# Optimization experiments

Measured on AMD Instinct MI355X. Metric: run time of the kernel, lower is better.

## Reference

```python
import jax, jax.numpy as jnp
import numpy as np

EMB = 512
HEADS = 8
HD = EMB // HEADS
DEPTH = 6
CONT = 100
CAT_DIMS = [100] * 28
CAT = len(CAT_DIMS)
HID = int(EMB * (4.0 / 3.0))  # 682, FT-Transformer ReGLU hidden
B = 128
OFFSETS = jnp.asarray(np.concatenate([[0], np.cumsum(CAT_DIMS[:-1])]).astype(np.int32))
SQRT_EMB = float(np.sqrt(EMB))  # scores are DIVIDED by emb**-0.5 in the source


def setup_inputs() -> dict:
    key = jax.random.key(0)
    ks = jax.random.split(key, 16)
    s = 0.02
    x_cat = jax.random.randint(ks[0], (B, CAT), 0, CAT_DIMS[0]).astype(jnp.float32)
    x_cont = jax.random.normal(ks[1], (B, CONT), dtype=jnp.float32)
    x = jnp.concatenate([x_cat, x_cont], axis=1)  # [B, CAT+CONT]
    return {
        "x": x,
        "tok_w": jax.random.normal(ks[2], (CONT + 1, EMB)) * s,
        "tok_b": jax.random.normal(ks[3], (CONT + CAT, EMB)) * s,
        "cat_emb": jax.random.normal(ks[4], (sum(CAT_DIMS), EMB)) * s,
        "Wqkv": jax.random.normal(ks[5], (DEPTH, EMB, 3 * EMB)) * s,
        "bqkv": jnp.zeros((DEPTH, 3 * EMB)),
        "Wout": jax.random.normal(ks[6], (DEPTH, EMB, EMB)) * s,
        "bout": jnp.zeros((DEPTH, EMB)),
        "W0": jax.random.normal(ks[7], (DEPTH, EMB, 2 * HID)) * s,
        "b0": jnp.zeros((DEPTH, 2 * HID)),
        "W1": jax.random.normal(ks[8], (DEPTH, HID, EMB)) * s,
        "b1": jnp.zeros((DEPTH, EMB)),
        "ln0_g": jnp.ones((DEPTH, EMB)),
        "ln0_b": jnp.zeros((DEPTH, EMB)),
        "ln1_g": jnp.ones((DEPTH, EMB)),
        "ln1_b": jnp.zeros((DEPTH, EMB)),
    }


def _ln(x, g, b):
    m = x.mean(-1, keepdims=True)
    v = x.var(-1, keepdims=True)
    return (x - m) / jnp.sqrt(v + 1e-5) * g + b


def _attn(x, Wqkv, bqkv, Wout, bout):
    Bn, S, _ = x.shape
    # faithful layout: reshape to (B,S,H,3*hd), move heads, chunk last dim
    qkv = (x @ Wqkv + bqkv).reshape(Bn, S, HEADS, 3 * HD).transpose(0, 2, 1, 3)
    q, k, v = jnp.split(qkv, 3, axis=-1)  # each [B,H,S,hd]
    scores = jnp.einsum("bhqd,bhkd->bhqk", q, k) * SQRT_EMB  # / (emb**-0.5)
    attn = jax.nn.softmax(jax.nn.softmax(scores, axis=-1), axis=-1)  # double softmax, as in source
    o = jnp.einsum("bhqk,bhkd->bhqd", attn, v)
    o = o.transpose(0, 2, 1, 3).reshape(Bn, S, EMB)
    return o @ Wout + bout


def _reglu(x):
    a, b = jnp.split(x, 2, axis=-1)
    return a * jax.nn.relu(b)


def _forward(x, tok_w, tok_b, cat_emb, Wqkv, bqkv, Wout, bout, W0, b0, W1, b1,
             ln0_g, ln0_b, ln1_g, ln1_b):
    # --- feature tokenizer ---
    x_cats = x[:, :CAT].astype(jnp.int32)
    x_conts = jnp.concatenate([jnp.ones((x.shape[0], 1), x.dtype), x[:, CAT:]], axis=1)  # [B, CONT+1]
    h = tok_w[None] * x_conts[:, :, None]  # [B, CONT+1, EMB]
    h = jnp.concatenate([h, cat_emb[x_cats + OFFSETS[None]]], axis=1)  # [B, S=129, EMB]
    bias = jnp.concatenate([jnp.zeros((1, EMB), h.dtype), tok_b], axis=0)
    h = h + bias[None]
    # --- transformer stack ---
    for i in range(DEPTH):
        xin = _ln(h, ln0_g[i], ln0_b[i]) if i else h  # layer 0 has no norm0
        h = h + _attn(xin, Wqkv[i], bqkv[i], Wout[i], bout[i])
        r = _ln(h, ln1_g[i], ln1_b[i])
        r = _reglu(r @ W0[i] + b0[i]) @ W1[i] + b1[i]
        h = h + r
    return h[:, 0]  # CLS token


def reference(x, tok_w, tok_b, cat_emb, Wqkv, bqkv, Wout, bout, W0, b0, W1, b1,
              ln0_g, ln0_b, ln1_g, ln1_b):
    return _forward(x, tok_w, tok_b, cat_emb, Wqkv, bqkv, Wout, bout, W0, b0, W1, b1,
                    ln0_g, ln0_b, ln1_g, ln1_b)
```

## Files before the change

### kernel.cpp

```cpp
#include <hip/hip_runtime.h>
#include <hip/hip_bf16.h>
#include <stdint.h>


typedef __hip_bfloat16 bf16_t;
typedef __attribute__((ext_vector_type(8))) __bf16 bf16x8;
typedef __attribute__((ext_vector_type(4))) __bf16 bf16x4;
typedef __attribute__((ext_vector_type(2))) __bf16 bf16x2;
typedef __attribute__((ext_vector_type(4))) float floatx4;

constexpr int M_ROWS = 16512;
constexpr float SQRT_EMB_F = 22.627416997969522f;

__device__ __forceinline__ floatx4 mfma16(bf16x8 a, bf16x8 b, floatx4 c) {
  return __builtin_amdgcn_mfma_f32_16x16x32_bf16(a, b, c, 0, 0, 0);
}

__device__ __forceinline__ void gload_lds16(const bf16_t* g, bf16_t* l) {
  __builtin_amdgcn_global_load_lds(
      (const __attribute__((address_space(1))) void*)g,
      (__attribute__((address_space(3))) void*)l, 16, 0, 0);
}

__device__ __forceinline__ size_t frag_chunk(int m, int k, int KT) {
  return ((size_t)(m >> 4) * KT + (k >> 5)) * 512 + (m & 15) * 8 + 128 * ((k >> 3) & 3);
}
__device__ __forceinline__ size_t frag_elem(int m, int k, int KT) {
  return frag_chunk(m, k, KT) + (k & 7);
}

template <int PERM>
__global__ __launch_bounds__(256) void transpose_cvt(const float* __restrict__ W,
    bf16_t* __restrict__ WT, int K, int N, int KP, int NP)
{
  __shared__ float tile[32][33];
  int k0 = blockIdx.x * 32, n0 = blockIdx.y * 32;
  const float* Wl = W + (size_t)blockIdx.z * K * N;
  bf16_t* WTl = WT + (size_t)blockIdx.z * NP * KP;
  const int KT = KP >> 5;
  #pragma unroll
  for (int r = 0; r < 32; r += 8) {
    int k = k0 + threadIdx.y + r, n = n0 + threadIdx.x;
    int srcn = PERM ? ((n & 1) ? 682 + (n >> 1) : (n >> 1)) : n;
    int valid = (k < K) && (PERM ? (n < 1364) : (n < N));
    tile[threadIdx.y + r][threadIdx.x] = valid ? Wl[(size_t)k * N + srcn] : 0.f;
  }
  __syncthreads();
  #pragma unroll
  for (int r = 0; r < 32; r += 8) {
    int n = n0 + threadIdx.y + r, k = k0 + threadIdx.x;
    if (n < NP && k < KP)
      WTl[frag_elem(n, k, KT)] = __float2bfloat16(tile[threadIdx.x][threadIdx.y + r]);
  }
}

__global__ __launch_bounds__(256) void tokenizer_kernel(const float* __restrict__ x,
    const float* __restrict__ tok_w, const float* __restrict__ tok_b,
    const float* __restrict__ cat_emb, float* __restrict__ h, bf16_t* __restrict__ ab)
{
  int row = blockIdx.x * 4 + (threadIdx.x >> 6);
  int lane = threadIdx.x & 63, e0 = lane * 8;
  int b = row / 129, t = row - b * 129;
  float v[8];
  if (t == 0) {
    #pragma unroll
    for (int u = 0; u < 8; u++) v[u] = tok_w[e0 + u];
  } else if (t <= 100) {
    float xv = x[(size_t)b * 128 + 28 + (t - 1)];
    const float* wp = tok_w + (size_t)t * 512 + e0;
    const float* bp = tok_b + (size_t)(t - 1) * 512 + e0;
    #pragma unroll
    for (int u = 0; u < 8; u++) v[u] = wp[u] * xv + bp[u];
  } else {
    int j = t - 101;
    int idx = (int)x[(size_t)b * 128 + j] + 100 * j;
    const float* cp = cat_emb + (size_t)idx * 512 + e0;
    const float* bp = tok_b + (size_t)(t - 1) * 512 + e0;
    #pragma unroll
    for (int u = 0; u < 8; u++) v[u] = cp[u] + bp[u];
  }
  float* hr = h + (size_t)row * 512 + e0;
  #pragma unroll
  for (int u = 0; u < 8; u++) hr[u] = v[u];
  bf16x8 o8;
  #pragma unroll
  for (int u = 0; u < 8; u++) o8[u] = (__bf16)__float2bfloat16(v[u]);
  *(bf16x8*)(ab + ((size_t)(row >> 4) * 16 + (lane >> 2)) * 512 + (row & 15) * 8 + 128 * (lane & 3)) = o8;
}

__global__ __launch_bounds__(256) void ln_kernel(const float* __restrict__ hin,
    bf16_t* __restrict__ out, const float* __restrict__ g, const float* __restrict__ bta)
{
  int row = blockIdx.x * 4 + (threadIdx.x >> 6);
  int lane = threadIdx.x & 63;
  const float* hr = hin + (size_t)row * 512 + lane * 8;
  float4 v0 = *(const float4*)hr;
  float4 v1 = *(const float4*)(hr + 4);
  float s = v0.x + v0.y + v0.z + v0.w + v1.x + v1.y + v1.z + v1.w;
  float q = v0.x * v0.x + v0.y * v0.y + v0.z * v0.z + v0.w * v0.w
          + v1.x * v1.x + v1.y * v1.y + v1.z * v1.z + v1.w * v1.w;
  #pragma unroll
  for (int o = 1; o < 64; o <<= 1) { s += __shfl_xor(s, o); q += __shfl_xor(q, o); }
  float mean = s * (1.f / 512.f);
  float var = q * (1.f / 512.f) - mean * mean;
  float rstd = rsqrtf(var + 1e-5f);
  float4 g0 = *(const float4*)(g + lane * 8);
  float4 g1 = *(const float4*)(g + lane * 8 + 4);
  float4 b0v = *(const float4*)(bta + lane * 8);
  float4 b1v = *(const float4*)(bta + lane * 8 + 4);
  bf16x8 o8;
  o8[0] = (__bf16)__float2bfloat16((v0.x - mean) * rstd * g0.x + b0v.x);
  o8[1] = (__bf16)__float2bfloat16((v0.y - mean) * rstd * g0.y + b0v.y);
  o8[2] = (__bf16)__float2bfloat16((v0.z - mean) * rstd * g0.z + b0v.z);
  o8[3] = (__bf16)__float2bfloat16((v0.w - mean) * rstd * g0.w + b0v.w);
  o8[4] = (__bf16)__float2bfloat16((v1.x - mean) * rstd * g1.x + b1v.x);
  o8[5] = (__bf16)__float2bfloat16((v1.y - mean) * rstd * g1.y + b1v.y);
  o8[6] = (__bf16)__float2bfloat16((v1.z - mean) * rstd * g1.z + b1v.z);
  o8[7] = (__bf16)__float2bfloat16((v1.w - mean) * rstd * g1.w + b1v.w);
  *(bf16x8*)(out + ((size_t)(row >> 4) * 16 + (lane >> 2)) * 512 + (row & 15) * 8 + 128 * (lane & 3)) = o8;
}

template <int MODE>
__global__ __launch_bounds__(256, 4) void gemm_frag(const bf16_t* __restrict__ A,
    const bf16_t* __restrict__ BT, const float* __restrict__ bias, int biasN,
    const float* __restrict__ resid, void* __restrict__ outp, int K, int N)
{
  __shared__ bf16_t lsA[2][8][512];
  __shared__ bf16_t lsB[2][8][512];

  const int total = gridDim.x * gridDim.y;
  const int lin = blockIdx.y * gridDim.x + blockIdx.x;
  const int xcd = lin & 7, kb2 = lin >> 3;
  const int qch = total >> 3, rch = total & 7;
  const int idx = xcd * qch + (xcd < rch ? xcd : rch) + kb2;
  const int bm = idx / gridDim.x;
  const int bn = idx - bm * gridDim.x;
  const int m0 = bm * 128, n0 = bn * 128;

  const int tid = threadIdx.x;
  const int w = tid >> 6, l = tid & 63, l15 = l & 15, quad = l >> 4;
  const int wm = (w >> 1) * 64, wn = (w & 1) * 64;
  const int KT = K >> 5;

  const bf16_t* gA0 = A  + ((size_t)((m0 >> 4) + 2 * w) * KT) * 512 + l * 8;
  const bf16_t* gA1 = gA0 + (size_t)KT * 512;
  const bf16_t* gB0 = BT + ((size_t)((n0 >> 4) + 2 * w) * KT) * 512 + l * 8;
  const bf16_t* gB1 = gB0 + (size_t)KT * 512;
  const int sa = w * 2;
  const int ra = (w >> 1) * 4;
  const int rb = (w & 1) * 4;

  auto stage = [&](int buf, int t) {
    const size_t go = (size_t)t * 512;
    gload_lds16(gA0 + go, &lsA[buf][sa][0]);
    gload_lds16(gA1 + go, &lsA[buf][sa + 1][0]);
    gload_lds16(gB0 + go, &lsB[buf][sa][0]);
    gload_lds16(gB1 + go, &lsB[buf][sa + 1][0]);
  };

  floatx4 z4 = {0.f, 0.f, 0.f, 0.f};
  floatx4 acc[4][4];
  #pragma unroll
  for (int i = 0; i < 4; i++)
    #pragma unroll
    for (int j = 0; j < 4; j++) acc[i][j] = z4;

  stage(0, 0);
  __syncthreads();

  int cur = 0;
  for (int t = 0; t < KT; ++t) {
    if (t + 1 < KT) stage(cur ^ 1, t + 1);
    bf16x8 af[4], bg[4];
    #pragma unroll
    for (int i = 0; i < 4; i++) {
      af[i] = *(const bf16x8*)&lsA[cur][ra + i][l * 8];
      bg[i] = *(const bf16x8*)&lsB[cur][rb + i][l * 8];
    }
    #pragma unroll
    for (int i = 0; i < 4; i++)
      #pragma unroll
      for (int j = 0; j < 4; j++)
        acc[i][j] = mfma16(bg[j], af[i], acc[i][j]);
    __syncthreads();
    cur ^= 1;
  }

  #pragma unroll
  for (int i = 0; i < 4; i++) {
    int m = m0 + wm + i * 16 + l15;
    #pragma unroll
    for (int j = 0; j < 4; j++) {
      int nb = n0 + wn + j * 16 + quad * 4;
      if (MODE == 2) {
        int c2b = nb >> 1;
        bf16x2 o2;
        #pragma unroll
        for (int u = 0; u < 2; u++) {
          int c2 = c2b + u;
          bool vld = (2 * c2 < biasN);
          float av = acc[i][j][2 * u]     + (vld ? bias[c2] : 0.f);
          float bv = acc[i][j][2 * u + 1] + (vld ? bias[682 + c2] : 0.f);
          o2[u] = (__bf16)__float2bfloat16(av * fmaxf(bv, 0.f));
        }
        *(bf16x2*)&((bf16_t*)outp)[frag_elem(m, c2b, (N >> 1) >> 5)] = o2;
      } else if (MODE == 1) {
        size_t idx2 = (size_t)m * N + nb;
        float4 rv = *(const float4*)(resid + idx2);
        float4 ov;
        ov.x = acc[i][j][0] + bias[nb + 0] + rv.x;
        ov.y = acc[i][j][1] + bias[nb + 1] + rv.y;
        ov.z = acc[i][j][2] + bias[nb + 2] + rv.z;
        ov.w = acc[i][j][3] + bias[nb + 3] + rv.w;
        *(float4*)((float*)outp + idx2) = ov;
      } else {
        bf16x4 o4;
        #pragma unroll
        for (int r = 0; r < 4; r++) {
          float bv = (nb + r < biasN) ? bias[nb + r] : 0.f;
          o4[r] = (__bf16)__float2bfloat16(acc[i][j][r] + bv);
        }
        *(bf16x4*)&((bf16_t*)outp)[frag_elem(m, nb, N >> 5)] = o4;
      }
    }
  }
}

constexpr int SP = 160;
__global__ __launch_bounds__(256) void attn_kernel(const bf16_t* __restrict__ qkv,
                                                   bf16_t* __restrict__ attnout)
{
  __shared__ bf16_t vt_lds[64 * SP];
  __shared__ float sc[32 * SP];
  bf16_t* p_lds = (bf16_t*)sc;
  __bf16* vt_raw = (__bf16*)vt_lds;

  const int bh = blockIdx.x, b = bh >> 3, hh = bh & 7;
  const int tid = threadIdx.x;
  const int w = tid >> 6, l = tid & 63, l15 = l & 15, quad = l >> 4;
  const int rbase = b * 129;

  for (int i = tid; i < SP * 64 / 2; i += 256) ((unsigned int*)vt_lds)[i] = 0u;
  __syncthreads();
  for (int c = tid; c < 129 * 8; c += 256) {
    int s = c >> 3, ch = c & 7;
    bf16x8 tv = *(const bf16x8*)(qkv + frag_chunk(rbase + s, hh * 192 + 128 + ch * 8, 48));
    #pragma unroll
    for (int j = 0; j < 8; j++) vt_raw[(size_t)(ch * 8 + j) * SP + s] = tv[j];
  }
  __syncthreads();

  for (int qt = 0; qt < 5; qt++) {
    bf16x8 zq = {};
    bf16x8 aq[2][2];
    #pragma unroll
    for (int mt = 0; mt < 2; mt++) {
      int m = qt * 32 + mt * 16 + l15;
      #pragma unroll
      for (int t = 0; t < 2; t++)
        aq[mt][t] = (m < 129)
            ? *(const bf16x8*)(qkv + frag_chunk(rbase + m, hh * 192 + t * 32 + quad * 8, 48)) : zq;
    }
    for (int nt = w; nt < 10; nt += 4) {
      int krow = nt * 16 + l15;
      floatx4 a0 = {0.f, 0.f, 0.f, 0.f}, a1 = {0.f, 0.f, 0.f, 0.f};
      #pragma unroll
      for (int t = 0; t < 2; t++) {
        bf16x8 kf = (krow < 129)
            ? *(const bf16x8*)(qkv + frag_chunk(rbase + krow, hh * 192 + 64 + t * 32 + quad * 8, 48))
            : zq;
        a0 = mfma16(aq[0][t], kf, a0);
        a1 = mfma16(aq[1][t], kf, a1);
      }
      #pragma unroll
      for (int r = 0; r < 4; r++) {
        sc[(quad * 4 + r) * SP + nt * 16 + l15]      = a0[r] * SQRT_EMB_F;
        sc[(16 + quad * 4 + r) * SP + nt * 16 + l15] = a1[r] * SQRT_EMB_F;
      }
    }
    __syncthreads();

    {
      int row = tid >> 3, sub = tid & 7;
      float vv[20];
      float mx = -1e30f;
      #pragma unroll
      for (int c = 0; c < 20; c++) {
        int j = sub + c * 8;
        vv[c] = (j < 129) ? sc[row * SP + j] : -1e30f;
        mx = fmaxf(mx, vv[c]);
      }
      #pragma unroll
      for (int o = 1; o < 8; o <<= 1) mx = fmaxf(mx, __shfl_xor(mx, o, 8));
      float sum = 0.f;
      #pragma unroll
      for (int c = 0; c < 20; c++) {
        int j = sub + c * 8;
        vv[c] = (j < 129) ? __expf(vv[c] - mx) : 0.f;
        sum += vv[c];
      }
      #pragma unroll
      for (int o = 1; o < 8; o <<= 1) sum += __shfl_xor(sum, o, 8);
      float inv = 1.f / sum;
      float mx2 = 0.f;
      #pragma unroll
      for (int c = 0; c < 20; c++) { vv[c] *= inv; mx2 = fmaxf(mx2, vv[c]); }
      #pragma unroll
      for (int o = 1; o < 8; o <<= 1) mx2 = fmaxf(mx2, __shfl_xor(mx2, o, 8));
      float sum2 = 0.f;
      #pragma unroll
      for (int c = 0; c < 20; c++) {
        int j = sub + c * 8;
        vv[c] = (j < 129) ? __expf(vv[c] - mx2) : 0.f;
        sum2 += vv[c];
      }
      #pragma unroll
      for (int o = 1; o < 8; o <<= 1) sum2 += __shfl_xor(sum2, o, 8);
      float inv2 = 1.f / sum2;
      __syncthreads();
      #pragma unroll
      for (int c = 0; c < 20; c++) {
        int j = sub + c * 8;
        p_lds[row * SP + j] = __float2bfloat16(vv[c] * inv2);
      }
    }
    __syncthreads();

    {
      int mt = w >> 1, nt0 = (w & 1) * 2;
      floatx4 oacc[2];
      oacc[0] = floatx4{0.f, 0.f, 0.f, 0.f};
      oacc[1] = floatx4{0.f, 0.f, 0.f, 0.f};
      #pragma unroll
      for (int t = 0; t < 5; t++) {
        bf16x8 pf = *(const bf16x8*)&p_lds[(mt * 16 + l15) * SP + t * 32 + quad * 8];
        #pragma unroll
        for (int n = 0; n < 2; n++) {
          bf16x8 vf = *(const bf16x8*)&vt_lds[((nt0 + n) * 16 + l15) * SP + t * 32 + quad * 8];
          oacc[n] = mfma16(pf, vf, oacc[n]);
        }
      }
      #pragma unroll
      for (int n = 0; n < 2; n++)
        #pragma unroll
        for (int r = 0; r < 4; r++) {
          int sq = qt * 32 + mt * 16 + quad * 4 + r;
          if (sq < 129) {
            int cc = hh * 64 + (nt0 + n) * 16 + l15;
            attnout[frag_elem(rbase + sq, cc, 16)] = __float2bfloat16(oacc[n][r]);
          }
        }
    }
    __syncthreads();
  }
}

__global__ __launch_bounds__(256) void out_copy(const float* __restrict__ h,
                                                float* __restrict__ out)
{
  int b = blockIdx.x, e = threadIdx.x;
  out[(size_t)b * 512 + e]       = h[(size_t)b * 129 * 512 + e];
  out[(size_t)b * 512 + e + 256] = h[(size_t)b * 129 * 512 + e + 256];
}

extern "C" void kernel_launch(void* const* d_in, const int* in_sizes, int n_in,
                              void* d_out, int out_size, void* d_ws, size_t ws_size,
                              hipStream_t stream)
{
  const float* x       = (const float*)d_in[0];
  const float* tok_w   = (const float*)d_in[1];
  const float* tok_b   = (const float*)d_in[2];
  const float* cat_emb = (const float*)d_in[3];
  const float* Wqkv    = (const float*)d_in[4];
  const float* bqkv    = (const float*)d_in[5];
  const float* Wout    = (const float*)d_in[6];
  const float* bout    = (const float*)d_in[7];
  const float* W0      = (const float*)d_in[8];
  const float* b0      = (const float*)d_in[9];
  const float* W1      = (const float*)d_in[10];
  const float* b1      = (const float*)d_in[11];
  const float* ln0_g   = (const float*)d_in[12];
  const float* ln0_b   = (const float*)d_in[13];
  const float* ln1_g   = (const float*)d_in[14];
  const float* ln1_b   = (const float*)d_in[15];

  size_t off = 0;
  char* base = (char*)d_ws;
  auto alloc = [&](size_t n) { char* p = base + off; off += (n + 255) & ~(size_t)255; return p; };
  float*  h     = (float*) alloc((size_t)M_ROWS * 512 * 4);
  bf16_t* ab    = (bf16_t*)alloc((size_t)M_ROWS * 512 * 2);
  bf16_t* qkv   = (bf16_t*)alloc((size_t)M_ROWS * 1536 * 2);
  bf16_t* attno = (bf16_t*)alloc((size_t)M_ROWS * 512 * 2);
  bf16_t* regl  = (bf16_t*)alloc((size_t)M_ROWS * 704 * 2);
  bf16_t* WqkvT = (bf16_t*)alloc((size_t)6 * 1536 * 512 * 2);
  bf16_t* WoutT = (bf16_t*)alloc((size_t)6 * 512 * 512 * 2);
  bf16_t* W0T   = (bf16_t*)alloc((size_t)6 * 1408 * 512 * 2);
  bf16_t* W1T   = (bf16_t*)alloc((size_t)6 * 512 * 704 * 2);
  (void)ws_size; (void)in_sizes; (void)n_in; (void)out_size;

  dim3 tb(32, 8, 1);
  transpose_cvt<0><<<dim3(16, 48, 6), tb, 0, stream>>>(Wqkv, WqkvT, 512, 1536, 512, 1536);
  transpose_cvt<0><<<dim3(16, 16, 6), tb, 0, stream>>>(Wout, WoutT, 512, 512, 512, 512);
  transpose_cvt<1><<<dim3(16, 44, 6), tb, 0, stream>>>(W0, W0T, 512, 1364, 512, 1408);
  transpose_cvt<0><<<dim3(22, 16, 6), tb, 0, stream>>>(W1, W1T, 682, 512, 704, 512);

  tokenizer_kernel<<<M_ROWS / 4, 256, 0, stream>>>(x, tok_w, tok_b, cat_emb, h, ab);

  for (int i = 0; i < 6; i++) {
    if (i)
      ln_kernel<<<M_ROWS / 4, 256, 0, stream>>>(h, ab, ln0_g + (size_t)i * 512,
                                                ln0_b + (size_t)i * 512);
    gemm_frag<0><<<dim3(12, 129), 256, 0, stream>>>(
        ab, WqkvT + (size_t)i * 1536 * 512, bqkv + (size_t)i * 1536, 1536, nullptr, qkv, 512, 1536);
    attn_kernel<<<1024, 256, 0, stream>>>(qkv, attno);
    gemm_frag<1><<<dim3(4, 129), 256, 0, stream>>>(
        attno, WoutT + (size_t)i * 512 * 512, bout + (size_t)i * 512, 512, h, h, 512, 512);
    ln_kernel<<<M_ROWS / 4, 256, 0, stream>>>(h, ab, ln1_g + (size_t)i * 512,
                                              ln1_b + (size_t)i * 512);
    gemm_frag<2><<<dim3(11, 129), 256, 0, stream>>>(
        ab, W0T + (size_t)i * 1408 * 512, b0 + (size_t)i * 1364, 1364, nullptr, regl, 512, 1408);
    gemm_frag<1><<<dim3(4, 129), 256, 0, stream>>>(
        regl, W1T + (size_t)i * 512 * 704, b1 + (size_t)i * 512, 512, h, h, 704, 512);
  }

  out_copy<<<128, 256, 0, stream>>>(h, (float*)d_out);
}
```

Before: 1.270 ms.

## Add 256x256-tile 8-wave GEMM with phased pipelining for QKV and FFN-up

Adds a gemm_big kernel with 256x256 output tiles, 512 threads, and a 64 KB double-buffered LDS stage. Each K step is split into four phases separated by explicit barriers and s_setprio around the MFMA groups, so global-to-LDS loads overlap with compute. The QKV and W0 (ReGLU) projections move to it, cutting the grid from 12x129/11x129 blocks to 6x65 and raising operand reuse per tile. To fit the larger tiles, buffers are padded to 16640 rows and W0/W1 are padded to 1536/768. This wastes some compute on padding columns and lowers occupancy.

```diff
diff --git a/kernel.cpp b/kernel.cpp
--- a/kernel.cpp
+++ b/kernel.cpp
@@ -10,6 +10,7 @@
 typedef __attribute__((ext_vector_type(4))) float floatx4;
 
 constexpr int M_ROWS = 16512;
+constexpr int MP_ROWS = 16640;
 constexpr float SQRT_EMB_F = 22.627416997969522f;
 
 __device__ __forceinline__ floatx4 mfma16(bf16x8 a, bf16x8 b, floatx4 c) {
@@ -20,6 +21,12 @@
   __builtin_amdgcn_global_load_lds(
       (const __attribute__((address_space(1))) void*)g,
       (__attribute__((address_space(3))) void*)l, 16, 0, 0);
+}
+
+__device__ __forceinline__ void phase_barrier() {
+  __builtin_amdgcn_sched_barrier(0);
+  __builtin_amdgcn_s_barrier();
+  __builtin_amdgcn_sched_barrier(0);
 }
 
 __device__ __forceinline__ size_t frag_chunk(int m, int k, int KT) {
@@ -121,12 +128,11 @@
 }
 
 template <int MODE>
-__global__ __launch_bounds__(256, 4) void gemm_frag(const bf16_t* __restrict__ A,
+__global__ __launch_bounds__(512, 2) void gemm_big(const bf16_t* __restrict__ A,
     const bf16_t* __restrict__ BT, const float* __restrict__ bias, int biasN,
-    const float* __restrict__ resid, void* __restrict__ outp, int K, int N)
-{
-  __shared__ bf16_t lsA[2][8][512];
-  __shared__ bf16_t lsB[2][8][512];
+    void* __restrict__ outp, int K, int N)
+{
+  __shared__ bf16_t ls[2][64][512];
 
   const int total = gridDim.x * gridDim.y;
   const int lin = blockIdx.y * gridDim.x + blockIdx.x;
@@ -135,65 +141,113 @@
   const int idx = xcd * qch + (xcd < rch ? xcd : rch) + kb2;
   const int bm = idx / gridDim.x;
   const int bn = idx - bm * gridDim.x;
-  const int m0 = bm * 128, n0 = bn * 128;
+  const int m0 = bm * 256, n0 = bn * 256;
 
   const int tid = threadIdx.x;
   const int w = tid >> 6, l = tid & 63, l15 = l & 15, quad = l >> 4;
-  const int wm = (w >> 1) * 64, wn = (w & 1) * 64;
-  const int KT = K >> 5;
-
-  const bf16_t* gA0 = A  + ((size_t)((m0 >> 4) + 2 * w) * KT) * 512 + l * 8;
-  const bf16_t* gA1 = gA0 + (size_t)KT * 512;
-  const bf16_t* gB0 = BT + ((size_t)((n0 >> 4) + 2 * w) * KT) * 512 + l * 8;
-  const bf16_t* gB1 = gB0 + (size_t)KT * 512;
-  const int sa = w * 2;
-  const int ra = (w >> 1) * 4;
-  const int rb = (w & 1) * 4;
-
-  auto stage = [&](int buf, int t) {
-    const size_t go = (size_t)t * 512;
-    gload_lds16(gA0 + go, &lsA[buf][sa][0]);
-    gload_lds16(gA1 + go, &lsA[buf][sa + 1][0]);
-    gload_lds16(gB0 + go, &lsB[buf][sa][0]);
-    gload_lds16(gB1 + go, &lsB[buf][sa + 1][0]);
+  const int wm = (w >> 2) * 128, wn = (w & 3) * 64;
+  const int KTg = K >> 5, KT2 = K >> 6;
+
+  const bf16_t* gsA[2];
+  const bf16_t* gsB[2];
+  #pragma unroll
+  for (int s = 0; s < 2; s++) {
+    gsA[s] = A  + ((size_t)((m0 >> 4) + 2 * w + s) * KTg) * 512 + l * 8;
+    gsB[s] = BT + ((size_t)((n0 >> 4) + 2 * w + s) * KTg) * 512 + l * 8;
+  }
+  const int caB = (2 * w) * 2;
+  const int cbB = 32 + (2 * w) * 2;
+  const int raB = wm >> 4;
+  const int rbB = wn >> 4;
+
+  auto stA = [&](int buf, int t, int kc) {
+    #pragma unroll
+    for (int s = 0; s < 2; s++)
+      gload_lds16(gsA[s] + (size_t)(t * 2 + kc) * 512, &ls[buf][caB + s * 2 + kc][0]);
   };
-
-  floatx4 z4 = {0.f, 0.f, 0.f, 0.f};
-  floatx4 acc[4][4];
-  #pragma unroll
-  for (int i = 0; i < 4; i++)
-    #pragma unroll
-    for (int j = 0; j < 4; j++) acc[i][j] = z4;
-
-  stage(0, 0);
-  __syncthreads();
-
+  auto stB = [&](int buf, int t, int kc) {
+    #pragma unroll
+    for (int s = 0; s < 2; s++)
+      gload_lds16(gsB[s] + (size_t)(t * 2 + kc) * 512, &ls[buf][cbB + s * 2 + kc][0]);
+  };
+
+  floatx4 acc[8][4];
+  #pragma unroll
+  for (int i = 0; i < 8; i++)
+    #pragma unroll
+    for (int j = 0; j < 4; j++) acc[i][j] = floatx4{0.f, 0.f, 0.f, 0.f};
+
+  stA(0, 0, 0); stB(0, 0, 0); stA(0, 0, 1); stB(0, 0, 1);
+  asm volatile("s_waitcnt vmcnt(4)" ::: "memory");
+  phase_barrier();
+
+  bf16x8 af[8], bg[4];
   int cur = 0;
-  for (int t = 0; t < KT; ++t) {
-    if (t + 1 < KT) stage(cur ^ 1, t + 1);
-    bf16x8 af[4], bg[4];
-    #pragma unroll
-    for (int i = 0; i < 4; i++) {
-      af[i] = *(const bf16x8*)&lsA[cur][ra + i][l * 8];
-      bg[i] = *(const bf16x8*)&lsB[cur][rb + i][l * 8];
-    }
+  for (int t = 0; t < KT2; ++t) {
+    const int nb = cur ^ 1;
+    const bool st = (t + 1 < KT2);
+    #pragma unroll
+    for (int i = 0; i < 4; i++) af[i] = *(const bf16x8*)&ls[cur][(raB + i) * 2 + 0][l * 8];
+    #pragma unroll
+    for (int j = 0; j < 4; j++) bg[j] = *(const bf16x8*)&ls[cur][32 + (rbB + j) * 2 + 0][l * 8];
+    if (st) stA(nb, t + 1, 0);
+    phase_barrier();
+    __builtin_amdgcn_s_setprio(1);
     #pragma unroll
     for (int i = 0; i < 4; i++)
       #pragma unroll
-      for (int j = 0; j < 4; j++)
-        acc[i][j] = mfma16(bg[j], af[i], acc[i][j]);
-    __syncthreads();
-    cur ^= 1;
-  }
-
-  #pragma unroll
-  for (int i = 0; i < 4; i++) {
+      for (int j = 0; j < 4; j++) acc[i][j] = mfma16(bg[j], af[i], acc[i][j]);
+    __builtin_amdgcn_s_setprio(0);
+    phase_barrier();
+    #pragma unroll
+    for (int i = 4; i < 8; i++) af[i] = *(const bf16x8*)&ls[cur][(raB + i) * 2 + 0][l * 8];
+    if (st) stB(nb, t + 1, 0);
+    phase_barrier();
+    __builtin_amdgcn_s_setprio(1);
+    #pragma unroll
+    for (int i = 4; i < 8; i++)
+      #pragma unroll
+      for (int j = 0; j < 4; j++) acc[i][j] = mfma16(bg[j], af[i], acc[i][j]);
+    __builtin_amdgcn_s_setprio(0);
+    if (st) asm volatile("s_waitcnt vmcnt(4)" ::: "memory");
+    else    asm volatile("s_waitcnt vmcnt(0)" ::: "memory");
+    phase_barrier();
+    #pragma unroll
+    for (int i = 0; i < 4; i++) af[i] = *(const bf16x8*)&ls[cur][(raB + i) * 2 + 1][l * 8];
+    #pragma unroll
+    for (int j = 0; j < 4; j++) bg[j] = *(const bf16x8*)&ls[cur][32 + (rbB + j) * 2 + 1][l * 8];
+    if (st) stA(nb, t + 1, 1);
+    phase_barrier();
+    __builtin_amdgcn_s_setprio(1);
+    #pragma unroll
+    for (int i = 0; i < 4; i++)
+      #pragma unroll
+      for (int j = 0; j < 4; j++) acc[i][j] = mfma16(bg[j], af[i], acc[i][j]);
+    __builtin_amdgcn_s_setprio(0);
+    phase_barrier();
+    #pragma unroll
+    for (int i = 4; i < 8; i++) af[i] = *(const bf16x8*)&ls[cur][(raB + i) * 2 + 1][l * 8];
+    if (st) stB(nb, t + 1, 1);
+    phase_barrier();
+    __builtin_amdgcn_s_setprio(1);
+    #pragma unroll
+    for (int i = 4; i < 8; i++)
+      #pragma unroll
+      for (int j = 0; j < 4; j++) acc[i][j] = mfma16(bg[j], af[i], acc[i][j]);
+    __builtin_amdgcn_s_setprio(0);
+    if (st) asm volatile("s_waitcnt vmcnt(4)" ::: "memory");
+    phase_barrier();
+    cur = nb;
+  }
+
+  #pragma unroll
+  for (int i = 0; i < 8; i++) {
     int m = m0 + wm + i * 16 + l15;
     #pragma unroll
     for (int j = 0; j < 4; j++) {
-      int nb = n0 + wn + j * 16 + quad * 4;
+      int nbc = n0 + wn + j * 16 + quad * 4;
       if (MODE == 2) {
-        int c2b = nb >> 1;
+        int c2b = nbc >> 1;
         bf16x2 o2;
         #pragma unroll
         for (int u = 0; u < 2; u++) {
@@ -204,7 +258,92 @@
           o2[u] = (__bf16)__float2bfloat16(av * fmaxf(bv, 0.f));
         }
         *(bf16x2*)&((bf16_t*)outp)[frag_elem(m, c2b, (N >> 1) >> 5)] = o2;
-      } else if (MODE == 1) {
+      } else {
+        bf16x4 o4;
+        #pragma unroll
+        for (int r = 0; r < 4; r++) {
+          float bv = (nbc + r < biasN) ? bias[nbc + r] : 0.f;
+          o4[r] = (__bf16)__float2bfloat16(acc[i][j][r] + bv);
+        }
+        *(bf16x4*)&((bf16_t*)outp)[frag_elem(m, nbc, N >> 5)] = o4;
+      }
+    }
+  }
+}
+
+template <int MODE>
+__global__ __launch_bounds__(256, 4) void gemm_frag(const bf16_t* __restrict__ A,
+    const bf16_t* __restrict__ BT, const float* __restrict__ bias, int biasN,
+    const float* __restrict__ resid, void* __restrict__ outp, int K, int N)
+{
+  __shared__ bf16_t lsA[2][8][512];
+  __shared__ bf16_t lsB[2][8][512];
+
+  const int total = gridDim.x * gridDim.y;
+  const int lin = blockIdx.y * gridDim.x + blockIdx.x;
+  const int xcd = lin & 7, kb2 = lin >> 3;
+  const int qch = total >> 3, rch = total & 7;
+  const int idx = xcd * qch + (xcd < rch ? xcd : rch) + kb2;
+  const int bm = idx / gridDim.x;
+  const int bn = idx - bm * gridDim.x;
+  const int m0 = bm * 128, n0 = bn * 128;
+
+  const int tid = threadIdx.x;
+  const int w = tid >> 6, l = tid & 63, l15 = l & 15, quad = l >> 4;
+  const int wm = (w >> 1) * 64, wn = (w & 1) * 64;
+  const int KT = K >> 5;
+
+  const bf16_t* gA0 = A  + ((size_t)((m0 >> 4) + 2 * w) * KT) * 512 + l * 8;
+  const bf16_t* gA1 = gA0 + (size_t)KT * 512;
+  const bf16_t* gB0 = BT + ((size_t)((n0 >> 4) + 2 * w) * KT) * 512 + l * 8;
+  const bf16_t* gB1 = gB0 + (size_t)KT * 512;
+  const int sa = w * 2;
+  const int ra = (w >> 1) * 4;
+  const int rb = (w & 1) * 4;
+
+  auto stage = [&](int buf, int t) {
+    const size_t go = (size_t)t * 512;
+    gload_lds16(gA0 + go, &lsA[buf][sa][0]);
+    gload_lds16(gA1 + go, &lsA[buf][sa + 1][0]);
+    gload_lds16(gB0 + go, &lsB[buf][sa][0]);
+    gload_lds16(gB1 + go, &lsB[buf][sa + 1][0]);
+  };
+
+  floatx4 z4 = {0.f, 0.f, 0.f, 0.f};
+  floatx4 acc[4][4];
+  #pragma unroll
+  for (int i = 0; i < 4; i++)
+    #pragma unroll
+    for (int j = 0; j < 4; j++) acc[i][j] = z4;
+
+  stage(0, 0);
+  __syncthreads();
+
+  int cur = 0;
+  for (int t = 0; t < KT; ++t) {
+    if (t + 1 < KT) stage(cur ^ 1, t + 1);
+    bf16x8 af[4], bg[4];
+    #pragma unroll
+    for (int i = 0; i < 4; i++) {
+      af[i] = *(const bf16x8*)&lsA[cur][ra + i][l * 8];
+      bg[i] = *(const bf16x8*)&lsB[cur][rb + i][l * 8];
+    }
+    #pragma unroll
+    for (int i = 0; i < 4; i++)
+      #pragma unroll
+      for (int j = 0; j < 4; j++)
+        acc[i][j] = mfma16(bg[j], af[i], acc[i][j]);
+    __syncthreads();
+    cur ^= 1;
+  }
+
+  #pragma unroll
+  for (int i = 0; i < 4; i++) {
+    int m = m0 + wm + i * 16 + l15;
+    #pragma unroll
+    for (int j = 0; j < 4; j++) {
+      int nb = n0 + wn + j * 16 + quad * 4;
+      if (MODE == 1) {
         size_t idx2 = (size_t)m * N + nb;
         float4 rv = *(const float4*)(resid + idx2);
         float4 ov;
@@ -387,22 +526,22 @@
   size_t off = 0;
   char* base = (char*)d_ws;
   auto alloc = [&](size_t n) { char* p = base + off; off += (n + 255) & ~(size_t)255; return p; };
-  float*  h     = (float*) alloc((size_t)M_ROWS * 512 * 4);
-  bf16_t* ab    = (bf16_t*)alloc((size_t)M_ROWS * 512 * 2);
-  bf16_t* qkv   = (bf16_t*)alloc((size_t)M_ROWS * 1536 * 2);
-  bf16_t* attno = (bf16_t*)alloc((size_t)M_ROWS * 512 * 2);
-  bf16_t* regl  = (bf16_t*)alloc((size_t)M_ROWS * 704 * 2);
+  float*  h     = (float*) alloc((size_t)MP_ROWS * 512 * 4);
+  bf16_t* ab    = (bf16_t*)alloc((size_t)MP_ROWS * 512 * 2);
+  bf16_t* qkv   = (bf16_t*)alloc((size_t)MP_ROWS * 1536 * 2);
+  bf16_t* attno = (bf16_t*)alloc((size_t)MP_ROWS * 512 * 2);
+  bf16_t* regl  = (bf16_t*)alloc((size_t)MP_ROWS * 768 * 2);
   bf16_t* WqkvT = (bf16_t*)alloc((size_t)6 * 1536 * 512 * 2);
   bf16_t* WoutT = (bf16_t*)alloc((size_t)6 * 512 * 512 * 2);
-  bf16_t* W0T   = (bf16_t*)alloc((size_t)6 * 1408 * 512 * 2);
-  bf16_t* W1T   = (bf16_t*)alloc((size_t)6 * 512 * 704 * 2);
+  bf16_t* W0T   = (bf16_t*)alloc((size_t)6 * 1536 * 512 * 2);
+  bf16_t* W1T   = (bf16_t*)alloc((size_t)6 * 512 * 768 * 2);
   (void)ws_size; (void)in_sizes; (void)n_in; (void)out_size;
 
   dim3 tb(32, 8, 1);
   transpose_cvt<0><<<dim3(16, 48, 6), tb, 0, stream>>>(Wqkv, WqkvT, 512, 1536, 512, 1536);
   transpose_cvt<0><<<dim3(16, 16, 6), tb, 0, stream>>>(Wout, WoutT, 512, 512, 512, 512);
-  transpose_cvt<1><<<dim3(16, 44, 6), tb, 0, stream>>>(W0, W0T, 512, 1364, 512, 1408);
-  transpose_cvt<0><<<dim3(22, 16, 6), tb, 0, stream>>>(W1, W1T, 682, 512, 704, 512);
+  transpose_cvt<1><<<dim3(16, 48, 6), tb, 0, stream>>>(W0, W0T, 512, 1364, 512, 1536);
+  transpose_cvt<0><<<dim3(24, 16, 6), tb, 0, stream>>>(W1, W1T, 682, 512, 768, 512);
 
   tokenizer_kernel<<<M_ROWS / 4, 256, 0, stream>>>(x, tok_w, tok_b, cat_emb, h, ab);
 
@@ -410,17 +549,17 @@
     if (i)
       ln_kernel<<<M_ROWS / 4, 256, 0, stream>>>(h, ab, ln0_g + (size_t)i * 512,
                                                 ln0_b + (size_t)i * 512);
-    gemm_frag<0><<<dim3(12, 129), 256, 0, stream>>>(
-        ab, WqkvT + (size_t)i * 1536 * 512, bqkv + (size_t)i * 1536, 1536, nullptr, qkv, 512, 1536);
+    gemm_big<0><<<dim3(6, 65), 512, 0, stream>>>(
+        ab, WqkvT + (size_t)i * 1536 * 512, bqkv + (size_t)i * 1536, 1536, qkv, 512, 1536);
     attn_kernel<<<1024, 256, 0, stream>>>(qkv, attno);
     gemm_frag<1><<<dim3(4, 129), 256, 0, stream>>>(
         attno, WoutT + (size_t)i * 512 * 512, bout + (size_t)i * 512, 512, h, h, 512, 512);
     ln_kernel<<<M_ROWS / 4, 256, 0, stream>>>(h, ab, ln1_g + (size_t)i * 512,
                                               ln1_b + (size_t)i * 512);
-    gemm_frag<2><<<dim3(11, 129), 256, 0, stream>>>(
-        ab, W0T + (size_t)i * 1408 * 512, b0 + (size_t)i * 1364, 1364, nullptr, regl, 512, 1408);
+    gemm_big<2><<<dim3(6, 65), 512, 0, stream>>>(
+        ab, W0T + (size_t)i * 1536 * 512, b0 + (size_t)i * 1364, 1364, regl, 512, 1536);
     gemm_frag<1><<<dim3(4, 129), 256, 0, stream>>>(
-        regl, W1T + (size_t)i * 512 * 704, b1 + (size_t)i * 512, 512, h, h, 704, 512);
+        regl, W1T + (size_t)i * 512 * 768, b1 + (size_t)i * 512, 512, h, h, 768, 512);
   }
 
   out_copy<<<128, 256, 0, stream>>>(h, (float*)d_out);
```

New measurement: 1.423 ms. 1.12x slower.
